# Optimization experiments

Measured on AMD Instinct MI355X. Metric: run time of the kernel, lower is better.

The kernel has to match this reference:

```python
import jax, jax.numpy as jnp
import numpy as np

D_MODEL = 512
N_HEADS = 8
D_FF = 1024
LV = 2048
LT = 512
GAMMA = 0.9
SCALE_BASE = 512  # XPOS default scale_base


def _dup_interleave(m):
    # (L, d/2) -> (L, d) duplicating each column: [a,b] -> [a,a,b,b]
    return jnp.repeat(m, 2, axis=-1)


def _xpos(x, downscale=False):
    # XPOS rotary embedding (RetNet-style), x: (B, L, d)
    B, L, d = x.shape
    half = d // 2
    s = (jnp.arange(0, d, 2, dtype=jnp.float32) + 0.4 * d) / (1.4 * d)  # (d/2,)
    scale = s[None, :] ** (jnp.arange(L, dtype=jnp.float32)[:, None] / SCALE_BASE)  # (L, d/2)
    inv_freq = 1.0 / (10000.0 ** (jnp.arange(half, dtype=jnp.float32) / half))
    ang = jnp.arange(L, dtype=jnp.float32)[:, None] * inv_freq[None, :]  # (L, d/2)
    if downscale:
        scale = 1.0 / scale
    sin = _dup_interleave(jnp.sin(ang) * scale)[None]  # (1, L, d)
    cos = _dup_interleave(jnp.cos(ang) * scale)[None]
    x1, x2 = x[..., 0::2], x[..., 1::2]
    rot = jnp.stack((-x2, x1), axis=-1).reshape(x.shape)  # rotate_every_two
    return x * cos + rot * sin


def _sine_pos(L, d):
    # DETR-style normalized 1D sine position embedding, mask = ones(1, L)
    x_embed = jnp.arange(1, L + 1, dtype=jnp.float32)  # cumsum of ones
    x_embed = x_embed / (x_embed[-1] + 1e-6) * (2.0 * np.pi)
    dim_t = jnp.arange(d, dtype=jnp.float32)
    dim_t = 10000.0 ** (2.0 * jnp.floor(dim_t / 2.0) / d)
    pos = x_embed[:, None] / dim_t[None, :]  # (L, d)
    pos = jnp.stack((jnp.sin(pos[:, 0::2]), jnp.cos(pos[:, 1::2])), axis=2).reshape(L, d)
    return pos[None]  # (1, L, d)


def _ln(x, w, b, eps=1e-5):
    mu = jnp.mean(x, axis=-1, keepdims=True)
    var = jnp.var(x, axis=-1, keepdims=True)
    return (x - mu) / jnp.sqrt(var + eps) * w + b


def _ret_forward(src_vid, src_txt, ln1_w, ln1_b, wq, bq, wk, bk, wv, bv, wo, bo,
                 lin1_w, lin1_b, lin2_w, lin2_b, ln2_w, ln2_b, ln3_w, ln3_b,
                 learn_ret_w):
    B, Lv, D = src_vid.shape
    Lt = src_txt.shape[1]
    h, dk = N_HEADS, D // N_HEADS

    # retention decay matrix D[n,m] = gamma^(n-m) for n>=m else 0
    n = jnp.arange(Lv)
    delta = jnp.maximum(n[:, None] - n[None, :], 0).astype(jnp.float32)
    Dm = jnp.where(n[:, None] >= n[None, :], GAMMA ** delta, 0.0)

    # learned sparse mask
    learn = jax.nn.sigmoid(learn_ret_w.reshape(Lv, Lv))
    diag = jnp.eye(Lv, dtype=jnp.float32)
    video_ret = (1.0 - diag) * learn
    learn_mask = diag + video_ret
    mask = Dm * learn_mask  # mask_choice == 'both'
    loss_sparsity = jnp.mean(jnp.abs(video_ret))

    # position encodings
    pos_vid_q = _xpos(src_vid)
    pos_vid_k = _xpos(src_vid, downscale=True)
    pos_txt = _sine_pos(Lt, D)
    src = jnp.concatenate([src_vid, src_txt], axis=1)       # (B, Lv+Lt, D)
    pos = jnp.concatenate([pos_vid_q, pos_txt], axis=1)
    pos_k = jnp.concatenate([pos_vid_k, pos_txt], axis=1)

    # --- RetLayer (eval mode: dropout = identity) ---
    src2 = _ln(src, ln1_w, ln1_b)
    q = src2[:, :Lv] + pos[:, :Lv]
    k = src2[:, :Lv] + pos_k[:, :Lv]
    v = src2[:, :Lv]

    # multi-head attention with MULTIPLICATIVE mask on logits
    qh = (q @ wq.T + bq).reshape(B, Lv, h, dk) / jnp.sqrt(jnp.float32(dk))
    kh = (k @ wk.T + bk).reshape(B, Lv, h, dk)
    vh = (v @ wv.T + bv).reshape(B, Lv, h, dk)
    attn = jnp.einsum('blhd,bmhd->bhlm', qh, kh) * mask[None, None]
    attn = jax.nn.softmax(attn, axis=-1)
    vid_att = jnp.einsum('bhlm,bmhd->blhd', attn, vh).reshape(B, Lv, D)
    vid_att = vid_att @ wo.T + bo

    src2 = jnp.concatenate([vid_att, src2[:, Lv:]], axis=1) + pos
    src = src + src2
    src2 = _ln(src, ln2_w, ln2_b)
    src2 = jax.nn.gelu(src2 @ lin1_w.T + lin1_b, approximate=False) @ lin2_w.T + lin2_b
    src = src + src2
    src = _ln(src, ln3_w, ln3_b)
    return src[:, :Lv], src[:, Lv:], loss_sparsity


def setup_inputs() -> dict:
    key = jax.random.key(0)
    ks = jax.random.split(key, 12)
    D, F = D_MODEL, D_FF
    w = lambda k, shp: (jax.random.normal(k, shp, dtype=jnp.float32) * 0.02)
    return {
        'src_vid': jax.random.normal(ks[0], (1, LV, D), dtype=jnp.float32),
        'src_txt': jax.random.normal(ks[1], (1, LT, D), dtype=jnp.float32),
        'ln1_w': jnp.ones((D,), jnp.float32), 'ln1_b': jnp.zeros((D,), jnp.float32),
        'wq': w(ks[2], (D, D)), 'bq': jnp.zeros((D,), jnp.float32),
        'wk': w(ks[3], (D, D)), 'bk': jnp.zeros((D,), jnp.float32),
        'wv': w(ks[4], (D, D)), 'bv': jnp.zeros((D,), jnp.float32),
        'wo': w(ks[5], (D, D)), 'bo': jnp.zeros((D,), jnp.float32),
        'lin1_w': w(ks[6], (F, D)), 'lin1_b': jnp.zeros((F,), jnp.float32),
        'lin2_w': w(ks[7], (D, F)), 'lin2_b': jnp.zeros((D,), jnp.float32),
        'ln2_w': jnp.ones((D,), jnp.float32), 'ln2_b': jnp.zeros((D,), jnp.float32),
        'ln3_w': jnp.ones((D,), jnp.float32), 'ln3_b': jnp.zeros((D,), jnp.float32),
        'learn_ret_w': jax.random.normal(ks[8], (LV * LV,), dtype=jnp.float32),
    }


def reference(src_vid, src_txt, ln1_w, ln1_b, wq, bq, wk, bk, wv, bv, wo, bo,
              lin1_w, lin1_b, lin2_w, lin2_b, ln2_w, ln2_b, ln3_w, ln3_b,
              learn_ret_w):
    return _ret_forward(src_vid, src_txt, ln1_w, ln1_b, wq, bq, wk, bk, wv, bv,
                        wo, bo, lin1_w, lin1_b, lin2_w, lin2_b, ln2_w, ln2_b,
                        ln3_w, ln3_b, learn_ret_w)
```

## Files before the change

kernel.cpp:

```cpp
#include <hip/hip_runtime.h>
#include <hip/hip_bf16.h>
#include <math.h>

#define LVID 2048
#define LTXT 512
#define DMOD 512
#define LTOT 2560
#define LOG2_GAMMA (-0.15200309344504995f)
#define LOG2E 1.4426950408889634f

typedef __bf16 bf16x8 __attribute__((ext_vector_type(8)));
typedef float f32x4 __attribute__((ext_vector_type(4)));

__device__ inline f32x4 mfma_bf16(bf16x8 a, bf16x8 b, f32x4 c) {
  return __builtin_amdgcn_mfma_f32_16x16x32_bf16(a, b, c, 0, 0, 0);
}

__device__ inline void gload_lds16(const void* g, void* l) {
  __builtin_amdgcn_global_load_lds(
      (const __attribute__((address_space(1))) void*)g,
      (__attribute__((address_space(3))) void*)l, 16, 0, 0);
}

union U8 { __hip_bfloat16 b[8]; uint4 u; };

__global__ __launch_bounds__(256) void k_prep(
    const float* __restrict__ lw, float* __restrict__ premask2,
    float* __restrict__ loss_out,
    const float* __restrict__ wq, const float* __restrict__ wk,
    const float* __restrict__ wv, const float* __restrict__ wo,
    const float* __restrict__ l1, const float* __restrict__ l2,
    __hip_bfloat16* __restrict__ dst) {
  int tid = threadIdx.x;
  if (blockIdx.x < 2048) {
    __shared__ float red[256];
    int idx0 = (blockIdx.x * 256 + tid) * 8;
    float s = 0.f;
#pragma unroll
    for (int e = 0; e < 8; e++) {
      int idx = idx0 + e;
      int i = idx >> 11, j = idx & 2047;
      float sig = 1.f / (1.f + expf(-lw[idx]));
      if (i != j) s += sig;
      float pm = (j > i) ? 0.f
               : ((j == i) ? 1.f : exp2f((float)(i - j) * LOG2_GAMMA) * sig);
      premask2[idx] = pm * LOG2E;
    }
    red[tid] = s; __syncthreads();
    for (int st = 128; st > 0; st >>= 1) { if (tid < st) red[tid] += red[tid + st]; __syncthreads(); }
    if (tid == 0) atomicAdd(loss_out, red[0] * (1.f / 4194304.f));
  } else {
    int i4 = (blockIdx.x - 2048) * 256 + tid;
    const float* sp; int base;
    if (i4 < 131072)      { if (i4 < 65536)  { sp = wq; base = 0; }      else { sp = wk; base = 65536; } }
    else if (i4 < 262144) { if (i4 < 196608) { sp = wv; base = 131072; } else { sp = wo; base = 196608; } }
    else if (i4 < 393216) { sp = l1; base = 262144; }
    else                  { sp = l2; base = 393216; }
    float4 v = ((const float4*)sp)[i4 - base];
    __hip_bfloat16 o[4] = {__float2bfloat16(v.x), __float2bfloat16(v.y),
                           __float2bfloat16(v.z), __float2bfloat16(v.w)};
    *(uint2*)(dst + (size_t)i4 * 4) = *(uint2*)o;
  }
}

__global__ __launch_bounds__(256) void k_ln1(
    const float* __restrict__ src_vid, const float* __restrict__ src_txt,
    const float* __restrict__ w, const float* __restrict__ b,
    __hip_bfloat16* __restrict__ acat, float* __restrict__ src2f,
    float* __restrict__ posb) {
  int row = blockIdx.x * 4 + (threadIdx.x >> 6);
  int lane = threadIdx.x & 63;
  const float* xs = (row < LVID) ? (src_vid + (size_t)row * DMOD)
                                 : (src_txt + (size_t)(row - LVID) * DMOD);
  float x[8];
  { float4 v0 = *(const float4*)&xs[lane * 8];
    float4 v1 = *(const float4*)&xs[lane * 8 + 4];
    x[0]=v0.x; x[1]=v0.y; x[2]=v0.z; x[3]=v0.w;
    x[4]=v1.x; x[5]=v1.y; x[6]=v1.z; x[7]=v1.w; }
  float s = 0.f;
#pragma unroll
  for (int i = 0; i < 8; i++) s += x[i];
#pragma unroll
  for (int st = 1; st < 64; st <<= 1) s += __shfl_xor(s, st, 64);
  float mu = s * (1.f / DMOD);
  float vs = 0.f;
#pragma unroll
  for (int i = 0; i < 8; i++) { float d = x[i] - mu; vs += d * d; }
#pragma unroll
  for (int st = 1; st < 64; st <<= 1) vs += __shfl_xor(vs, st, 64);
  float inv = rsqrtf(vs * (1.f / DMOD) + 1e-5f);
  float y[8];
  { float4 w0 = *(const float4*)&w[lane * 8];
    float4 w1 = *(const float4*)&w[lane * 8 + 4];
    float4 b0 = *(const float4*)&b[lane * 8];
    float4 b1 = *(const float4*)&b[lane * 8 + 4];
    float wv_[8] = {w0.x,w0.y,w0.z,w0.w,w1.x,w1.y,w1.z,w1.w};
    float bv_[8] = {b0.x,b0.y,b0.z,b0.w,b1.x,b1.y,b1.z,b1.w};
#pragma unroll
    for (int i = 0; i < 8; i++) y[i] = (x[i] - mu) * inv * wv_[i] + bv_[i]; }
  size_t base = (size_t)row * DMOD + lane * 8;
  if (row < LVID) {
    U8 pv;
#pragma unroll
    for (int i = 0; i < 8; i++) pv.b[i] = __float2bfloat16(y[i]);
    *(uint4*)&acat[(size_t)(4096 + row) * DMOD + lane * 8] = pv.u;
    float pq[8], pk[8];
    float l = (float)row;
#pragma unroll
    for (int p = 0; p < 4; p++) {
      int j = lane * 4 + p;
      float sj = (2.f * j + 204.8f) * (1.f / 716.8f);
      float scale = powf(sj, l * (1.f / 512.f));
      float invfreq = powf(10000.f, -(float)j * (1.f / 256.f));
      float sn, cs; sincosf(l * invfreq, &sn, &cs);
      float cq = cs * scale, sq = sn * scale;
      pq[2*p]   = x[2*p] * cq - x[2*p+1] * sq;
      pq[2*p+1] = x[2*p+1] * cq + x[2*p] * sq;
      float isc = 1.f / scale;
      float ck = cs * isc, sk = sn * isc;
      pk[2*p]   = x[2*p] * ck - x[2*p+1] * sk;
      pk[2*p+1] = x[2*p+1] * ck + x[2*p] * sk;
    }
    *(float4*)&posb[base]     = *(float4*)&pq[0];
    *(float4*)&posb[base + 4] = *(float4*)&pq[4];
    U8 pqv, pkv;
#pragma unroll
    for (int i = 0; i < 8; i++) {
      pqv.b[i] = __float2bfloat16(y[i] + pq[i]);
      pkv.b[i] = __float2bfloat16(y[i] + pk[i]);
    }
    *(uint4*)&acat[(size_t)row * DMOD + lane * 8] = pqv.u;
    *(uint4*)&acat[(size_t)(2048 + row) * DMOD + lane * 8] = pkv.u;
  } else {
    *(float4*)&src2f[base]     = *(float4*)&y[0];
    *(float4*)&src2f[base + 4] = *(float4*)&y[4];
    int l = row - LVID;
    float xe = (float)(l + 1) * (6.28318530717958647692f / 512.000001f);
    float ps[8];
#pragma unroll
    for (int p = 0; p < 4; p++) {
      int j = lane * 4 + p;
      float dimt = powf(10000.f, (float)j * (1.f / 256.f));
      float a = xe / dimt;
      ps[2*p] = sinf(a); ps[2*p+1] = cosf(a);
    }
    *(float4*)&posb[base]     = *(float4*)&ps[0];
    *(float4*)&posb[base + 4] = *(float4*)&ps[4];
  }
}

__global__ __launch_bounds__(256) void k_ln2(
    const float* __restrict__ src_txt, const float* __restrict__ src2f,
    const float* __restrict__ posb, float* __restrict__ srcA,
    const float* __restrict__ w, const float* __restrict__ b,
    __hip_bfloat16* __restrict__ obf) {
  int row = blockIdx.x * 4 + (threadIdx.x >> 6);
  int lane = threadIdx.x & 63;
  size_t base = (size_t)row * DMOD + lane * 8;
  float x[8];
  if (row < LVID) {
    float4 v0 = *(const float4*)&srcA[base];
    float4 v1 = *(const float4*)&srcA[base + 4];
    x[0]=v0.x; x[1]=v0.y; x[2]=v0.z; x[3]=v0.w;
    x[4]=v1.x; x[5]=v1.y; x[6]=v1.z; x[7]=v1.w;
  } else {
    size_t tb = (size_t)(row - LVID) * DMOD + lane * 8;
#pragma unroll
    for (int i = 0; i < 8; i++) x[i] = src_txt[tb + i] + src2f[base + i] + posb[base + i];
    *(float4*)&srcA[base]     = *(float4*)&x[0];
    *(float4*)&srcA[base + 4] = *(float4*)&x[4];
  }
  float s = 0.f;
#pragma unroll
  for (int i = 0; i < 8; i++) s += x[i];
#pragma unroll
  for (int st = 1; st < 64; st <<= 1) s += __shfl_xor(s, st, 64);
  float mu = s * (1.f / DMOD);
  float vs = 0.f;
#pragma unroll
  for (int i = 0; i < 8; i++) { float d = x[i] - mu; vs += d * d; }
#pragma unroll
  for (int st = 1; st < 64; st <<= 1) vs += __shfl_xor(vs, st, 64);
  float inv = rsqrtf(vs * (1.f / DMOD) + 1e-5f);
  float4 w0 = *(const float4*)&w[lane * 8];
  float4 w1 = *(const float4*)&w[lane * 8 + 4];
  float4 b0 = *(const float4*)&b[lane * 8];
  float4 b1 = *(const float4*)&b[lane * 8 + 4];
  float wv_[8] = {w0.x,w0.y,w0.z,w0.w,w1.x,w1.y,w1.z,w1.w};
  float bv_[8] = {b0.x,b0.y,b0.z,b0.w,b1.x,b1.y,b1.z,b1.w};
  U8 o;
#pragma unroll
  for (int i = 0; i < 8; i++)
    o.b[i] = __float2bfloat16((x[i] - mu) * inv * wv_[i] + bv_[i]);
  *(uint4*)&obf[base] = o.u;
}

__global__ __launch_bounds__(256) void k_ln3(
    const float* __restrict__ srcA, const float* __restrict__ ffo,
    const float* __restrict__ w, const float* __restrict__ b,
    float* __restrict__ o) {
  int row = blockIdx.x * 4 + (threadIdx.x >> 6);
  int lane = threadIdx.x & 63;
  size_t base = (size_t)row * DMOD + lane * 8;
  float x[8];
  { float4 a0 = *(const float4*)&srcA[base];
    float4 a1 = *(const float4*)&srcA[base + 4];
    float4 f0 = *(const float4*)&ffo[base];
    float4 f1 = *(const float4*)&ffo[base + 4];
    x[0]=a0.x+f0.x; x[1]=a0.y+f0.y; x[2]=a0.z+f0.z; x[3]=a0.w+f0.w;
    x[4]=a1.x+f1.x; x[5]=a1.y+f1.y; x[6]=a1.z+f1.z; x[7]=a1.w+f1.w; }
  float s = 0.f;
#pragma unroll
  for (int i = 0; i < 8; i++) s += x[i];
#pragma unroll
  for (int st = 1; st < 64; st <<= 1) s += __shfl_xor(s, st, 64);
  float mu = s * (1.f / DMOD);
  float vs = 0.f;
#pragma unroll
  for (int i = 0; i < 8; i++) { float d = x[i] - mu; vs += d * d; }
#pragma unroll
  for (int st = 1; st < 64; st <<= 1) vs += __shfl_xor(vs, st, 64);
  float inv = rsqrtf(vs * (1.f / DMOD) + 1e-5f);
  float4 w0 = *(const float4*)&w[lane * 8];
  float4 w1 = *(const float4*)&w[lane * 8 + 4];
  float4 b0 = *(const float4*)&b[lane * 8];
  float4 b1 = *(const float4*)&b[lane * 8 + 4];
  float wv_[8] = {w0.x,w0.y,w0.z,w0.w,w1.x,w1.y,w1.z,w1.w};
  float bv_[8] = {b0.x,b0.y,b0.z,b0.w,b1.x,b1.y,b1.z,b1.w};
  float y[8];
#pragma unroll
  for (int i = 0; i < 8; i++) y[i] = (x[i] - mu) * inv * wv_[i] + bv_[i];
  *(float4*)&o[base]     = *(float4*)&y[0];
  *(float4*)&o[base + 4] = *(float4*)&y[4];
}

template <int EPI>
__global__ __launch_bounds__(256) void k_gemm2(
    const __hip_bfloat16* __restrict__ A, const __hip_bfloat16* __restrict__ W0,
    const float* __restrict__ b0, const float* __restrict__ b1,
    const float* __restrict__ b2, void* __restrict__ Cv,
    const float* __restrict__ res1, const float* __restrict__ res2,
    float* __restrict__ vtot, int M, int N, int K) {
  __shared__ __hip_bfloat16 sA[2][4096];
  __shared__ __hip_bfloat16 sB[2][4096];
  int tid = threadIdx.x, lane = tid & 63, w = tid >> 6;
  int c16 = lane & 15, q4 = lane >> 4;
  int bm = blockIdx.y * 64, bn = blockIdx.x * 64;
  int seg = (EPI == 3) ? (bm >> 11) : 0;
  const __hip_bfloat16* Wp = (EPI == 3) ? (W0 + (size_t)seg * N * K) : W0;
  int srow = tid >> 2, scol = (tid & 3) * 8;
  const __hip_bfloat16* gA = A + (size_t)(bm + srow) * K + scol;
  const __hip_bfloat16* gB = Wp + (size_t)(bn + srow) * K + scol;
  auto stage = [&](int buf, int k0) {
    gload_lds16(gA + k0,      &sA[buf][0]    + (size_t)tid * 8);
    gload_lds16(gA + k0 + 32, &sA[buf][2048] + (size_t)tid * 8);
    gload_lds16(gB + k0,      &sB[buf][0]    + (size_t)tid * 8);
    gload_lds16(gB + k0 + 32, &sB[buf][2048] + (size_t)tid * 8);
  };
  f32x4 acc[2][2];
  { f32x4 z = {0.f,0.f,0.f,0.f}; acc[0][0]=z; acc[0][1]=z; acc[1][0]=z; acc[1][1]=z; }
  int wm = w & 1, wn = w >> 1;
  const int S = K >> 6;
  stage(0, 0);
  for (int s = 0; s < S; s++) {
    __syncthreads();
    if (s + 1 < S) stage((s + 1) & 1, (s + 1) * 64);
    int bf = s & 1;
#pragma unroll
    for (int kc = 0; kc < 2; kc++) {
      bf16x8 a0  = *(const bf16x8*)&sA[bf][kc*2048 + (wm*32 + c16)*32 + q4*8];
      bf16x8 a1  = *(const bf16x8*)&sA[bf][kc*2048 + (wm*32 + 16 + c16)*32 + q4*8];
      bf16x8 bv0 = *(const bf16x8*)&sB[bf][kc*2048 + (wn*32 + c16)*32 + q4*8];
      bf16x8 bv1 = *(const bf16x8*)&sB[bf][kc*2048 + (wn*32 + 16 + c16)*32 + q4*8];
      acc[0][0] = mfma_bf16(a0, bv0, acc[0][0]);
      acc[0][1] = mfma_bf16(a0, bv1, acc[0][1]);
      acc[1][0] = mfma_bf16(a1, bv0, acc[1][0]);
      acc[1][1] = mfma_bf16(a1, bv1, acc[1][1]);
    }
  }
  float alpha = (EPI == 3 && seg == 0) ? 0.125f : 1.f;
  const float* bp = (EPI == 3) ? (seg == 0 ? b0 : (seg == 1 ? b1 : b2)) : b0;
  float vsum[2] = {0.f, 0.f};
#pragma unroll
  for (int t = 0; t < 2; t++) {
#pragma unroll
    for (int u = 0; u < 2; u++) {
      int n = bn + wn*32 + u*16 + c16;
      float bs = bp[n];
#pragma unroll
      for (int r = 0; r < 4; r++) {
        int m = bm + wm*32 + t*16 + q4*4 + r;
        float v = (acc[t][u][r] + bs) * alpha;
        if (EPI == 4) v = 0.5f * v * (1.f + erff(v * 0.70710678118654752f));
        if (EPI == 0) {
          ((float*)Cv)[(size_t)m * N + n] = v;
        } else if (EPI == 1 || EPI == 4) {
          ((__hip_bfloat16*)Cv)[(size_t)m * N + n] = __float2bfloat16(v);
        } else if (EPI == 2) {
          size_t off = (size_t)m * N + n;
          ((float*)Cv)[off] = v + res1[off] + res2[off];
        } else {
          __hip_bfloat16 vb = __float2bfloat16(v);
          ((__hip_bfloat16*)Cv)[(size_t)(m & 2047) * 1536 + seg * 512 + n] = vb;
          if (seg == 2) vsum[u] += __bfloat162float(vb);
        }
      }
    }
  }
  if (EPI == 3 && seg == 2) {
#pragma unroll
    for (int u = 0; u < 2; u++) {
      float s2 = vsum[u];
      s2 += __shfl_xor(s2, 16, 64);
      s2 += __shfl_xor(s2, 32, 64);
      if (q4 == 0) atomicAdd(&vtot[bn + wn*32 + u*16 + c16], s2);
    }
  }
}

__global__ __launch_bounds__(256) void k_attn(
    const __hip_bfloat16* __restrict__ qkv,
    const float* __restrict__ premask2,
    const float* __restrict__ Vtot,
    __hip_bfloat16* __restrict__ outp) {
  __shared__ __hip_bfloat16 sQ[64][72];
  __shared__ __hip_bfloat16 sK[2][64][72];
  __shared__ __hip_bfloat16 sVt[2][64][72];
  __shared__ __hip_bfloat16 sP[64][72];
  __shared__ float sVa[4][64];
  int i0 = blockIdx.x * 64, h = blockIdx.y;
  int tid = threadIdx.x, lane = tid & 63, w = tid >> 6;
  int c16 = lane & 15, q4 = lane >> 4;
  {
    int r = tid >> 2, c0 = (tid & 3) * 16;
    const __hip_bfloat16* g = qkv + (size_t)(i0 + r) * 1536 + h * 64 + c0;
    *(uint4*)&sQ[r][c0]     = *(const uint4*)g;
    *(uint4*)&sQ[r][c0 + 8] = *(const uint4*)(g + 8);
  }
  int thi = i0 >> 6;
  int tlo = (i0 > 900) ? ((i0 - 900) >> 6) : 0;
  float rm = 0.f, rz = 0.f;
  f32x4 O[4];
  { f32x4 z = {0.f,0.f,0.f,0.f}; O[0]=z; O[1]=z; O[2]=z; O[3]=z; }
  float vacc = 0.f;
  int kr = tid >> 2, kc = (tid & 3) * 16;
  uint4 pk0, pk1;
  U8 pv0, pv1;
  {
    const __hip_bfloat16* gk = qkv + (size_t)(tlo*64 + kr) * 1536 + 512 + h*64 + kc;
    pk0 = *(const uint4*)gk; pk1 = *(const uint4*)(gk + 8);
    const __hip_bfloat16* gv = qkv + (size_t)(tlo*64 + w*16) * 1536 + 1024 + h*64 + lane;
#pragma unroll
    for (int j = 0; j < 8; j++) pv0.b[j] = gv[(size_t)j * 1536];
#pragma unroll
    for (int j = 0; j < 8; j++) pv1.b[j] = gv[(size_t)(j + 8) * 1536];
  }
  for (int t = tlo; t <= thi; t++) {
    int buf = (t - tlo) & 1;
    *(uint4*)&sK[buf][kr][kc]       = pk0;
    *(uint4*)&sK[buf][kr][kc + 8]   = pk1;
    *(uint4*)&sVt[buf][lane][w*16]     = pv0.u;
    *(uint4*)&sVt[buf][lane][w*16 + 8] = pv1.u;
#pragma unroll
    for (int j = 0; j < 8; j++) vacc += __bfloat162float(pv0.b[j]);
#pragma unroll
    for (int j = 0; j < 8; j++) vacc += __bfloat162float(pv1.b[j]);
    __syncthreads();
    if (t < thi) {
      const __hip_bfloat16* gk = qkv + (size_t)((t+1)*64 + kr) * 1536 + 512 + h*64 + kc;
      pk0 = *(const uint4*)gk; pk1 = *(const uint4*)(gk + 8);
      const __hip_bfloat16* gv = qkv + (size_t)((t+1)*64 + w*16) * 1536 + 1024 + h*64 + lane;
#pragma unroll
      for (int j = 0; j < 8; j++) pv0.b[j] = gv[(size_t)j * 1536];
#pragma unroll
      for (int j = 0; j < 8; j++) pv1.b[j] = gv[(size_t)(j + 8) * 1536];
    }
    bf16x8 bq0 = *(const bf16x8*)&sQ[w*16 + c16][q4*8];
    bf16x8 bq1 = *(const bf16x8*)&sQ[w*16 + c16][32 + q4*8];
    f32x4 St[4];
#pragma unroll
    for (int jt = 0; jt < 4; jt++) {
      f32x4 z = {0.f,0.f,0.f,0.f};
      bf16x8 a0 = *(const bf16x8*)&sK[buf][jt*16 + c16][q4*8];
      bf16x8 a1 = *(const bf16x8*)&sK[buf][jt*16 + c16][32 + q4*8];
      z = mfma_bf16(a0, bq0, z);
      z = mfma_bf16(a1, bq1, z);
      St[jt] = z;
    }
    int qg = i0 + w*16 + c16;
    float lg[4][4];
    float tmax = -3.0e38f;
#pragma unroll
    for (int jt = 0; jt < 4; jt++) {
      float4 pm = *(const float4*)&premask2[(size_t)qg * 2048 + t*64 + jt*16 + q4*4];
      lg[jt][0] = St[jt][0] * pm.x; lg[jt][1] = St[jt][1] * pm.y;
      lg[jt][2] = St[jt][2] * pm.z; lg[jt][3] = St[jt][3] * pm.w;
#pragma unroll
      for (int r = 0; r < 4; r++) tmax = fmaxf(tmax, lg[jt][r]);
    }
    tmax = fmaxf(tmax, __shfl_xor(tmax, 16, 64));
    tmax = fmaxf(tmax, __shfl_xor(tmax, 32, 64));
    float mn = fmaxf(rm, tmax);
    float al = exp2f(rm - mn);
    rm = mn;
    float zp = 0.f;
#pragma unroll
    for (int jt = 0; jt < 4; jt++) {
      U8 e4;
      float e0 = exp2f(lg[jt][0] - rm), e1 = exp2f(lg[jt][1] - rm);
      float e2 = exp2f(lg[jt][2] - rm), e3 = exp2f(lg[jt][3] - rm);
      zp += e0 + e1 + e2 + e3;
      e4.b[0] = __float2bfloat16(e0); e4.b[1] = __float2bfloat16(e1);
      e4.b[2] = __float2bfloat16(e2); e4.b[3] = __float2bfloat16(e3);
      *(uint2*)&sP[w*16 + c16][jt*16 + q4*4] = *(uint2*)&e4.b[0];
    }
    zp += __shfl_xor(zp, 16, 64);
    zp += __shfl_xor(zp, 32, 64);
    rz = rz * al + zp;
    float alr[4];
#pragma unroll
    for (int r = 0; r < 4; r++) alr[r] = __shfl(al, q4*4 + r, 64);
#pragma unroll
    for (int dt = 0; dt < 4; dt++)
#pragma unroll
      for (int r = 0; r < 4; r++) O[dt][r] *= alr[r];
    bf16x8 ap0 = *(const bf16x8*)&sP[w*16 + c16][q4*8];
    bf16x8 ap1 = *(const bf16x8*)&sP[w*16 + c16][32 + q4*8];
#pragma unroll
    for (int dt = 0; dt < 4; dt++) {
      bf16x8 bv0 = *(const bf16x8*)&sVt[buf][dt*16 + c16][q4*8];
      bf16x8 bv1 = *(const bf16x8*)&sVt[buf][dt*16 + c16][32 + q4*8];
      O[dt] = mfma_bf16(ap0, bv0, O[dt]);
      O[dt] = mfma_bf16(ap1, bv1, O[dt]);
    }
  }
  sVa[w][lane] = vacc;
  __syncthreads();
  float rmr[4], rzr[4];
#pragma unroll
  for (int r = 0; r < 4; r++) {
    rmr[r] = __shfl(rm, q4*4 + r, 64);
    rzr[r] = __shfl(rz, q4*4 + r, 64);
  }
  float nu = (float)(2048 - 64 * (thi - tlo + 1));
#pragma unroll
  for (int dt = 0; dt < 4; dt++) {
    int d = dt*16 + c16;
    float va = sVa[0][d] + sVa[1][d] + sVa[2][d] + sVa[3][d];
    float vu = Vtot[h*64 + d] - va;
#pragma unroll
    for (int r = 0; r < 4; r++) {
      float eu = exp2f(-rmr[r]);
      float o = (O[dt][r] + eu * vu) / (rzr[r] + nu * eu);
      outp[(size_t)(i0 + w*16 + q4*4 + r) * DMOD + h*64 + d] = __float2bfloat16(o);
    }
  }
}

extern "C" void kernel_launch(void* const* d_in, const int* in_sizes, int n_in,
                              void* d_out, int out_size, void* d_ws, size_t ws_size,
                              hipStream_t stream) {
  const float* src_vid = (const float*)d_in[0];
  const float* src_txt = (const float*)d_in[1];
  const float* ln1_w = (const float*)d_in[2];
  const float* ln1_b = (const float*)d_in[3];
  const float* wq = (const float*)d_in[4];
  const float* bq = (const float*)d_in[5];
  const float* wk = (const float*)d_in[6];
  const float* bk = (const float*)d_in[7];
  const float* wv = (const float*)d_in[8];
  const float* bv = (const float*)d_in[9];
  const float* wo = (const float*)d_in[10];
  const float* bo = (const float*)d_in[11];
  const float* lin1_w = (const float*)d_in[12];
  const float* lin1_b = (const float*)d_in[13];
  const float* lin2_w = (const float*)d_in[14];
  const float* lin2_b = (const float*)d_in[15];
  const float* ln2_w = (const float*)d_in[16];
  const float* ln2_b = (const float*)d_in[17];
  const float* ln3_w = (const float*)d_in[18];
  const float* ln3_b = (const float*)d_in[19];
  const float* lw = (const float*)d_in[20];
  float* out = (float*)d_out;

  char* wsb = (char*)d_ws;
  float* premask2       = (float*)(wsb + 0);
  __hip_bfloat16* wqb   = (__hip_bfloat16*)(wsb + 16777216);
  __hip_bfloat16* wob   = wqb + 786432;
  __hip_bfloat16* l1b   = wqb + 1048576;
  __hip_bfloat16* l2b   = wqb + 1572864;
  __hip_bfloat16* acat  = (__hip_bfloat16*)(wsb + 20971520);
  __hip_bfloat16* qkvb  = (__hip_bfloat16*)(wsb + 27262976);
  __hip_bfloat16* vattb = (__hip_bfloat16*)(wsb + 33554432);
  float* srcA           = (float*)(wsb + 35651584);
  float* src2f          = (float*)(wsb + 40894464);
  float* posb           = (float*)(wsb + 46137344);
  __hip_bfloat16* s2b   = (__hip_bfloat16*)(wsb + 51380224);
  __hip_bfloat16* hidb  = (__hip_bfloat16*)(wsb + 54525952);
  float* ffo            = (float*)(wsb + 59768832);
  float* Vtot           = (float*)(wsb + 65011712);

  hipMemsetAsync(out + 1310720, 0, sizeof(float), stream);
  hipMemsetAsync(Vtot, 0, 512 * sizeof(float), stream);

  k_prep<<<4096, 256, 0, stream>>>(lw, premask2, out + 1310720,
                                   wq, wk, wv, wo, lin1_w, lin2_w, wqb);
  k_ln1<<<640, 256, 0, stream>>>(src_vid, src_txt, ln1_w, ln1_b,
                                 acat, src2f, posb);
  k_gemm2<3><<<dim3(8, 96), 256, 0, stream>>>(acat, wqb, bq, bk, bv,
      qkvb, nullptr, nullptr, Vtot, 6144, 512, 512);
  k_attn<<<dim3(32, 8), 256, 0, stream>>>(qkvb, premask2, Vtot, vattb);
  k_gemm2<2><<<dim3(8, 32), 256, 0, stream>>>(vattb, wob, bo, nullptr, nullptr,
      srcA, src_vid, posb, nullptr, 2048, 512, 512);
  k_ln2<<<640, 256, 0, stream>>>(src_txt, src2f, posb, srcA, ln2_w, ln2_b, s2b);
  k_gemm2<4><<<dim3(16, 40), 256, 0, stream>>>(s2b, l1b, lin1_b, nullptr, nullptr,
      hidb, nullptr, nullptr, nullptr, 2560, 1024, 512);
  k_gemm2<0><<<dim3(8, 40), 256, 0, stream>>>(hidb, l2b, lin2_b, nullptr, nullptr,
      ffo, nullptr, nullptr, nullptr, 2560, 512, 1024);
  k_ln3<<<640, 256, 0, stream>>>(srcA, ffo, ln3_w, ln3_b, out);
}
```

Baseline: 238.3 us.

## Enlarge GEMM tiles to 128x128, fuse prep with LN1, use fast math

The GEMM block tile grows from 64x64 to 128x128 with a 4x4 MFMA accumulator per wave and a k-step of 32, so each staged fragment is reused more and fewer blocks are launched. The prep and LN1 kernels are merged into one launch, and the loss is accumulated in workspace and copied to the output in LN3, which removes one memset. Transcendentals switch to fast intrinsics (__expf, __powf, __sincosf). The risks are low occupancy from grids of only 64-192 blocks on a large GPU, more register pressure, and lower accuracy in the positional terms.

```diff
diff --git a/kernel.cpp b/kernel.cpp
--- a/kernel.cpp
+++ b/kernel.cpp
@@ -24,23 +24,28 @@
 
 union U8 { __hip_bfloat16 b[8]; uint4 u; };
 
-__global__ __launch_bounds__(256) void k_prep(
+__global__ __launch_bounds__(256) void k_prep_ln1(
     const float* __restrict__ lw, float* __restrict__ premask2,
-    float* __restrict__ loss_out,
+    float* __restrict__ lossws,
     const float* __restrict__ wq, const float* __restrict__ wk,
     const float* __restrict__ wv, const float* __restrict__ wo,
     const float* __restrict__ l1, const float* __restrict__ l2,
-    __hip_bfloat16* __restrict__ dst) {
+    __hip_bfloat16* __restrict__ dst,
+    const float* __restrict__ src_vid, const float* __restrict__ src_txt,
+    const float* __restrict__ w, const float* __restrict__ b,
+    __hip_bfloat16* __restrict__ acat, float* __restrict__ src2f,
+    float* __restrict__ posb) {
   int tid = threadIdx.x;
-  if (blockIdx.x < 2048) {
+  int blk = blockIdx.x;
+  if (blk < 2048) {
     __shared__ float red[256];
-    int idx0 = (blockIdx.x * 256 + tid) * 8;
+    int idx0 = (blk * 256 + tid) * 8;
     float s = 0.f;
 #pragma unroll
     for (int e = 0; e < 8; e++) {
       int idx = idx0 + e;
       int i = idx >> 11, j = idx & 2047;
-      float sig = 1.f / (1.f + expf(-lw[idx]));
+      float sig = 1.f / (1.f + __expf(-lw[idx]));
       if (i != j) s += sig;
       float pm = (j > i) ? 0.f
                : ((j == i) ? 1.f : exp2f((float)(i - j) * LOG2_GAMMA) * sig);
@@ -48,9 +53,9 @@
     }
     red[tid] = s; __syncthreads();
     for (int st = 128; st > 0; st >>= 1) { if (tid < st) red[tid] += red[tid + st]; __syncthreads(); }
-    if (tid == 0) atomicAdd(loss_out, red[0] * (1.f / 4194304.f));
-  } else {
-    int i4 = (blockIdx.x - 2048) * 256 + tid;
+    if (tid == 0) atomicAdd(lossws, red[0] * (1.f / 4194304.f));
+  } else if (blk < 4096) {
+    int i4 = (blk - 2048) * 256 + tid;
     const float* sp; int base;
     if (i4 < 131072)      { if (i4 < 65536)  { sp = wq; base = 0; }      else { sp = wk; base = 65536; } }
     else if (i4 < 262144) { if (i4 < 196608) { sp = wv; base = 131072; } else { sp = wo; base = 196608; } }
@@ -60,92 +65,86 @@
     __hip_bfloat16 o[4] = {__float2bfloat16(v.x), __float2bfloat16(v.y),
                            __float2bfloat16(v.z), __float2bfloat16(v.w)};
     *(uint2*)(dst + (size_t)i4 * 4) = *(uint2*)o;
-  }
-}
-
-__global__ __launch_bounds__(256) void k_ln1(
-    const float* __restrict__ src_vid, const float* __restrict__ src_txt,
-    const float* __restrict__ w, const float* __restrict__ b,
-    __hip_bfloat16* __restrict__ acat, float* __restrict__ src2f,
-    float* __restrict__ posb) {
-  int row = blockIdx.x * 4 + (threadIdx.x >> 6);
-  int lane = threadIdx.x & 63;
-  const float* xs = (row < LVID) ? (src_vid + (size_t)row * DMOD)
-                                 : (src_txt + (size_t)(row - LVID) * DMOD);
-  float x[8];
-  { float4 v0 = *(const float4*)&xs[lane * 8];
-    float4 v1 = *(const float4*)&xs[lane * 8 + 4];
-    x[0]=v0.x; x[1]=v0.y; x[2]=v0.z; x[3]=v0.w;
-    x[4]=v1.x; x[5]=v1.y; x[6]=v1.z; x[7]=v1.w; }
-  float s = 0.f;
-#pragma unroll
-  for (int i = 0; i < 8; i++) s += x[i];
-#pragma unroll
-  for (int st = 1; st < 64; st <<= 1) s += __shfl_xor(s, st, 64);
-  float mu = s * (1.f / DMOD);
-  float vs = 0.f;
-#pragma unroll
-  for (int i = 0; i < 8; i++) { float d = x[i] - mu; vs += d * d; }
-#pragma unroll
-  for (int st = 1; st < 64; st <<= 1) vs += __shfl_xor(vs, st, 64);
-  float inv = rsqrtf(vs * (1.f / DMOD) + 1e-5f);
-  float y[8];
-  { float4 w0 = *(const float4*)&w[lane * 8];
-    float4 w1 = *(const float4*)&w[lane * 8 + 4];
-    float4 b0 = *(const float4*)&b[lane * 8];
-    float4 b1 = *(const float4*)&b[lane * 8 + 4];
-    float wv_[8] = {w0.x,w0.y,w0.z,w0.w,w1.x,w1.y,w1.z,w1.w};
-    float bv_[8] = {b0.x,b0.y,b0.z,b0.w,b1.x,b1.y,b1.z,b1.w};
-#pragma unroll
-    for (int i = 0; i < 8; i++) y[i] = (x[i] - mu) * inv * wv_[i] + bv_[i]; }
-  size_t base = (size_t)row * DMOD + lane * 8;
-  if (row < LVID) {
-    U8 pv;
-#pragma unroll
-    for (int i = 0; i < 8; i++) pv.b[i] = __float2bfloat16(y[i]);
-    *(uint4*)&acat[(size_t)(4096 + row) * DMOD + lane * 8] = pv.u;
-    float pq[8], pk[8];
-    float l = (float)row;
-#pragma unroll
-    for (int p = 0; p < 4; p++) {
-      int j = lane * 4 + p;
-      float sj = (2.f * j + 204.8f) * (1.f / 716.8f);
-      float scale = powf(sj, l * (1.f / 512.f));
-      float invfreq = powf(10000.f, -(float)j * (1.f / 256.f));
-      float sn, cs; sincosf(l * invfreq, &sn, &cs);
-      float cq = cs * scale, sq = sn * scale;
-      pq[2*p]   = x[2*p] * cq - x[2*p+1] * sq;
-      pq[2*p+1] = x[2*p+1] * cq + x[2*p] * sq;
-      float isc = 1.f / scale;
-      float ck = cs * isc, sk = sn * isc;
-      pk[2*p]   = x[2*p] * ck - x[2*p+1] * sk;
-      pk[2*p+1] = x[2*p+1] * ck + x[2*p] * sk;
-    }
-    *(float4*)&posb[base]     = *(float4*)&pq[0];
-    *(float4*)&posb[base + 4] = *(float4*)&pq[4];
-    U8 pqv, pkv;
-#pragma unroll
-    for (int i = 0; i < 8; i++) {
-      pqv.b[i] = __float2bfloat16(y[i] + pq[i]);
-      pkv.b[i] = __float2bfloat16(y[i] + pk[i]);
-    }
-    *(uint4*)&acat[(size_t)row * DMOD + lane * 8] = pqv.u;
-    *(uint4*)&acat[(size_t)(2048 + row) * DMOD + lane * 8] = pkv.u;
   } else {
-    *(float4*)&src2f[base]     = *(float4*)&y[0];
-    *(float4*)&src2f[base + 4] = *(float4*)&y[4];
-    int l = row - LVID;
-    float xe = (float)(l + 1) * (6.28318530717958647692f / 512.000001f);
-    float ps[8];
-#pragma unroll
-    for (int p = 0; p < 4; p++) {
-      int j = lane * 4 + p;
-      float dimt = powf(10000.f, (float)j * (1.f / 256.f));
-      float a = xe / dimt;
-      ps[2*p] = sinf(a); ps[2*p+1] = cosf(a);
-    }
-    *(float4*)&posb[base]     = *(float4*)&ps[0];
-    *(float4*)&posb[base + 4] = *(float4*)&ps[4];
+    int row = (blk - 4096) * 4 + (tid >> 6);
+    int lane = tid & 63;
+    const float* xs = (row < LVID) ? (src_vid + (size_t)row * DMOD)
+                                   : (src_txt + (size_t)(row - LVID) * DMOD);
+    float x[8];
+    { float4 v0 = *(const float4*)&xs[lane * 8];
+      float4 v1 = *(const float4*)&xs[lane * 8 + 4];
+      x[0]=v0.x; x[1]=v0.y; x[2]=v0.z; x[3]=v0.w;
+      x[4]=v1.x; x[5]=v1.y; x[6]=v1.z; x[7]=v1.w; }
+    float s = 0.f;
+#pragma unroll
+    for (int i = 0; i < 8; i++) s += x[i];
+#pragma unroll
+    for (int st = 1; st < 64; st <<= 1) s += __shfl_xor(s, st, 64);
+    float mu = s * (1.f / DMOD);
+    float vs = 0.f;
+#pragma unroll
+    for (int i = 0; i < 8; i++) { float d = x[i] - mu; vs += d * d; }
+#pragma unroll
+    for (int st = 1; st < 64; st <<= 1) vs += __shfl_xor(vs, st, 64);
+    float inv = rsqrtf(vs * (1.f / DMOD) + 1e-5f);
+    float y[8];
+    { float4 w0 = *(const float4*)&w[lane * 8];
+      float4 w1 = *(const float4*)&w[lane * 8 + 4];
+      float4 b0 = *(const float4*)&b[lane * 8];
+      float4 b1 = *(const float4*)&b[lane * 8 + 4];
+      float wv_[8] = {w0.x,w0.y,w0.z,w0.w,w1.x,w1.y,w1.z,w1.w};
+      float bv_[8] = {b0.x,b0.y,b0.z,b0.w,b1.x,b1.y,b1.z,b1.w};
+#pragma unroll
+      for (int i = 0; i < 8; i++) y[i] = (x[i] - mu) * inv * wv_[i] + bv_[i]; }
+    size_t base = (size_t)row * DMOD + lane * 8;
+    if (row < LVID) {
+      U8 pv;
+#pragma unroll
+      for (int i = 0; i < 8; i++) pv.b[i] = __float2bfloat16(y[i]);
+      *(uint4*)&acat[(size_t)(4096 + row) * DMOD + lane * 8] = pv.u;
+      float pq[8], pk[8];
+      float l = (float)row;
+#pragma unroll
+      for (int p = 0; p < 4; p++) {
+        int j = lane * 4 + p;
+        float sj = (2.f * j + 204.8f) * (1.f / 716.8f);
+        float scale = __powf(sj, l * (1.f / 512.f));
+        float invfreq = __powf(10000.f, -(float)j * (1.f / 256.f));
+        float sn, cs; __sincosf(l * invfreq, &sn, &cs);
+        float cq = cs * scale, sq = sn * scale;
+        pq[2*p]   = x[2*p] * cq - x[2*p+1] * sq;
+        pq[2*p+1] = x[2*p+1] * cq + x[2*p] * sq;
+        float isc = 1.f / scale;
+        float ck = cs * isc, sk = sn * isc;
+        pk[2*p]   = x[2*p] * ck - x[2*p+1] * sk;
+        pk[2*p+1] = x[2*p+1] * ck + x[2*p] * sk;
+      }
+      *(float4*)&posb[base]     = *(float4*)&pq[0];
+      *(float4*)&posb[base + 4] = *(float4*)&pq[4];
+      U8 pqv, pkv;
+#pragma unroll
+      for (int i = 0; i < 8; i++) {
+        pqv.b[i] = __float2bfloat16(y[i] + pq[i]);
+        pkv.b[i] = __float2bfloat16(y[i] + pk[i]);
+      }
+      *(uint4*)&acat[(size_t)row * DMOD + lane * 8] = pqv.u;
+      *(uint4*)&acat[(size_t)(2048 + row) * DMOD + lane * 8] = pkv.u;
+    } else {
+      *(float4*)&src2f[base]     = *(float4*)&y[0];
+      *(float4*)&src2f[base + 4] = *(float4*)&y[4];
+      int l = row - LVID;
+      float xe = (float)(l + 1) * (6.28318530717958647692f / 512.000001f);
+      float ps[8];
+#pragma unroll
+      for (int p = 0; p < 4; p++) {
+        int j = lane * 4 + p;
+        float dimt = __powf(10000.f, (float)j * (1.f / 256.f));
+        float a = xe / dimt;
+        ps[2*p] = __sinf(a); ps[2*p+1] = __cosf(a);
+      }
+      *(float4*)&posb[base]     = *(float4*)&ps[0];
+      *(float4*)&posb[base + 4] = *(float4*)&ps[4];
+    }
   }
 }
 
@@ -198,7 +197,8 @@
 __global__ __launch_bounds__(256) void k_ln3(
     const float* __restrict__ srcA, const float* __restrict__ ffo,
     const float* __restrict__ w, const float* __restrict__ b,
-    float* __restrict__ o) {
+    float* __restrict__ o, const float* __restrict__ lossws) {
+  if (blockIdx.x == 0 && threadIdx.x == 0) o[1310720] = lossws[0];
   int row = blockIdx.x * 4 + (threadIdx.x >> 6);
   int lane = threadIdx.x & 63;
   size_t base = (size_t)row * DMOD + lane * 8;
@@ -235,7 +235,7 @@
 }
 
 template <int EPI>
-__global__ __launch_bounds__(256) void k_gemm2(
+__global__ __launch_bounds__(256) void k_gemm3(
     const __hip_bfloat16* __restrict__ A, const __hip_bfloat16* __restrict__ W0,
     const float* __restrict__ b0, const float* __restrict__ b1,
     const float* __restrict__ b2, void* __restrict__ Cv,
@@ -245,75 +245,82 @@
   __shared__ __hip_bfloat16 sB[2][4096];
   int tid = threadIdx.x, lane = tid & 63, w = tid >> 6;
   int c16 = lane & 15, q4 = lane >> 4;
-  int bm = blockIdx.y * 64, bn = blockIdx.x * 64;
+  int bm = blockIdx.y * 128, bn = blockIdx.x * 128;
   int seg = (EPI == 3) ? (bm >> 11) : 0;
-  const __hip_bfloat16* Wp = (EPI == 3) ? (W0 + (size_t)seg * N * K) : W0;
-  int srow = tid >> 2, scol = (tid & 3) * 8;
-  const __hip_bfloat16* gA = A + (size_t)(bm + srow) * K + scol;
-  const __hip_bfloat16* gB = Wp + (size_t)(bn + srow) * K + scol;
+  const __hip_bfloat16* Wp = (EPI == 3) ? (W0 + (size_t)seg * ((size_t)N * K)) : W0;
+  int r0 = tid >> 2, cc0 = (tid & 3) * 8;
+  const __hip_bfloat16* gA0 = A  + (size_t)(bm + r0) * K + cc0;
+  const __hip_bfloat16* gA1 = A  + (size_t)(bm + 64 + r0) * K + cc0;
+  const __hip_bfloat16* gB0 = Wp + (size_t)(bn + r0) * K + cc0;
+  const __hip_bfloat16* gB1 = Wp + (size_t)(bn + 64 + r0) * K + cc0;
   auto stage = [&](int buf, int k0) {
-    gload_lds16(gA + k0,      &sA[buf][0]    + (size_t)tid * 8);
-    gload_lds16(gA + k0 + 32, &sA[buf][2048] + (size_t)tid * 8);
-    gload_lds16(gB + k0,      &sB[buf][0]    + (size_t)tid * 8);
-    gload_lds16(gB + k0 + 32, &sB[buf][2048] + (size_t)tid * 8);
+    gload_lds16(gA0 + k0, &sA[buf][(size_t)tid * 8]);
+    gload_lds16(gA1 + k0, &sA[buf][2048 + (size_t)tid * 8]);
+    gload_lds16(gB0 + k0, &sB[buf][(size_t)tid * 8]);
+    gload_lds16(gB1 + k0, &sB[buf][2048 + (size_t)tid * 8]);
   };
-  f32x4 acc[2][2];
-  { f32x4 z = {0.f,0.f,0.f,0.f}; acc[0][0]=z; acc[0][1]=z; acc[1][0]=z; acc[1][1]=z; }
+  f32x4 acc[4][4];
+  { f32x4 z = {0.f,0.f,0.f,0.f};
+#pragma unroll
+    for (int i = 0; i < 4; i++)
+#pragma unroll
+      for (int j = 0; j < 4; j++) acc[i][j] = z; }
   int wm = w & 1, wn = w >> 1;
-  const int S = K >> 6;
+  const int S = K >> 5;
   stage(0, 0);
   for (int s = 0; s < S; s++) {
     __syncthreads();
-    if (s + 1 < S) stage((s + 1) & 1, (s + 1) * 64);
+    if (s + 1 < S) stage((s + 1) & 1, (s + 1) * 32);
     int bf = s & 1;
-#pragma unroll
-    for (int kc = 0; kc < 2; kc++) {
-      bf16x8 a0  = *(const bf16x8*)&sA[bf][kc*2048 + (wm*32 + c16)*32 + q4*8];
-      bf16x8 a1  = *(const bf16x8*)&sA[bf][kc*2048 + (wm*32 + 16 + c16)*32 + q4*8];
-      bf16x8 bv0 = *(const bf16x8*)&sB[bf][kc*2048 + (wn*32 + c16)*32 + q4*8];
-      bf16x8 bv1 = *(const bf16x8*)&sB[bf][kc*2048 + (wn*32 + 16 + c16)*32 + q4*8];
-      acc[0][0] = mfma_bf16(a0, bv0, acc[0][0]);
-      acc[0][1] = mfma_bf16(a0, bv1, acc[0][1]);
-      acc[1][0] = mfma_bf16(a1, bv0, acc[1][0]);
-      acc[1][1] = mfma_bf16(a1, bv1, acc[1][1]);
-    }
+    bf16x8 af[4], bfr[4];
+#pragma unroll
+    for (int i = 0; i < 4; i++)
+      af[i] = *(const bf16x8*)&sA[bf][(wm*64 + i*16 + c16) * 32 + q4*8];
+#pragma unroll
+    for (int j = 0; j < 4; j++)
+      bfr[j] = *(const bf16x8*)&sB[bf][(wn*64 + j*16 + c16) * 32 + q4*8];
+#pragma unroll
+    for (int i = 0; i < 4; i++)
+#pragma unroll
+      for (int j = 0; j < 4; j++)
+        acc[i][j] = mfma_bf16(af[i], bfr[j], acc[i][j]);
   }
   float alpha = (EPI == 3 && seg == 0) ? 0.125f : 1.f;
   const float* bp = (EPI == 3) ? (seg == 0 ? b0 : (seg == 1 ? b1 : b2)) : b0;
-  float vsum[2] = {0.f, 0.f};
-#pragma unroll
-  for (int t = 0; t < 2; t++) {
-#pragma unroll
-    for (int u = 0; u < 2; u++) {
-      int n = bn + wn*32 + u*16 + c16;
-      float bs = bp[n];
+  float vsum[4] = {0.f, 0.f, 0.f, 0.f};
+#pragma unroll
+  for (int j = 0; j < 4; j++) {
+    int n = bn + wn*64 + j*16 + c16;
+    float bs = bp[n];
+#pragma unroll
+    for (int i = 0; i < 4; i++) {
 #pragma unroll
       for (int r = 0; r < 4; r++) {
-        int m = bm + wm*32 + t*16 + q4*4 + r;
-        float v = (acc[t][u][r] + bs) * alpha;
+        int m = bm + wm*64 + i*16 + q4*4 + r;
+        float v = (acc[i][j][r] + bs) * alpha;
         if (EPI == 4) v = 0.5f * v * (1.f + erff(v * 0.70710678118654752f));
         if (EPI == 0) {
           ((float*)Cv)[(size_t)m * N + n] = v;
-        } else if (EPI == 1 || EPI == 4) {
-          ((__hip_bfloat16*)Cv)[(size_t)m * N + n] = __float2bfloat16(v);
         } else if (EPI == 2) {
           size_t off = (size_t)m * N + n;
           ((float*)Cv)[off] = v + res1[off] + res2[off];
+        } else if (EPI == 4) {
+          ((__hip_bfloat16*)Cv)[(size_t)m * N + n] = __float2bfloat16(v);
         } else {
           __hip_bfloat16 vb = __float2bfloat16(v);
           ((__hip_bfloat16*)Cv)[(size_t)(m & 2047) * 1536 + seg * 512 + n] = vb;
-          if (seg == 2) vsum[u] += __bfloat162float(vb);
+          if (seg == 2) vsum[j] += __bfloat162float(vb);
         }
       }
     }
   }
   if (EPI == 3 && seg == 2) {
 #pragma unroll
-    for (int u = 0; u < 2; u++) {
-      float s2 = vsum[u];
+    for (int j = 0; j < 4; j++) {
+      float s2 = vsum[j];
       s2 += __shfl_xor(s2, 16, 64);
       s2 += __shfl_xor(s2, 32, 64);
-      if (q4 == 0) atomicAdd(&vtot[bn + wn*32 + u*16 + c16], s2);
+      if (q4 == 0) atomicAdd(&vtot[bn + wn*64 + j*16 + c16], s2);
     }
   }
 }
@@ -499,23 +506,23 @@
   __hip_bfloat16* hidb  = (__hip_bfloat16*)(wsb + 54525952);
   float* ffo            = (float*)(wsb + 59768832);
   float* Vtot           = (float*)(wsb + 65011712);
-
-  hipMemsetAsync(out + 1310720, 0, sizeof(float), stream);
-  hipMemsetAsync(Vtot, 0, 512 * sizeof(float), stream);
-
-  k_prep<<<4096, 256, 0, stream>>>(lw, premask2, out + 1310720,
-                                   wq, wk, wv, wo, lin1_w, lin2_w, wqb);
-  k_ln1<<<640, 256, 0, stream>>>(src_vid, src_txt, ln1_w, ln1_b,
-                                 acat, src2f, posb);
-  k_gemm2<3><<<dim3(8, 96), 256, 0, stream>>>(acat, wqb, bq, bk, bv,
+  float* lossws         = Vtot + 512;
+
+  hipMemsetAsync(Vtot, 0, 513 * sizeof(float), stream);
+
+  k_prep_ln1<<<4736, 256, 0, stream>>>(lw, premask2, lossws,
+      wq, wk, wv, wo, lin1_w, lin2_w, wqb,
+      src_vid, src_txt, ln1_w, ln1_b, acat, src2f, posb);
+
+  k_gemm3<3><<<dim3(4, 48), 256, 0, stream>>>(acat, wqb, bq, bk, bv,
       qkvb, nullptr, nullptr, Vtot, 6144, 512, 512);
   k_attn<<<dim3(32, 8), 256, 0, stream>>>(qkvb, premask2, Vtot, vattb);
-  k_gemm2<2><<<dim3(8, 32), 256, 0, stream>>>(vattb, wob, bo, nullptr, nullptr,
+  k_gemm3<2><<<dim3(4, 16), 256, 0, stream>>>(vattb, wob, bo, nullptr, nullptr,
       srcA, src_vid, posb, nullptr, 2048, 512, 512);
   k_ln2<<<640, 256, 0, stream>>>(src_txt, src2f, posb, srcA, ln2_w, ln2_b, s2b);
-  k_gemm2<4><<<dim3(16, 40), 256, 0, stream>>>(s2b, l1b, lin1_b, nullptr, nullptr,
+  k_gemm3<4><<<dim3(8, 20), 256, 0, stream>>>(s2b, l1b, lin1_b, nullptr, nullptr,
       hidb, nullptr, nullptr, nullptr, 2560, 1024, 512);
-  k_gemm2<0><<<dim3(8, 40), 256, 0, stream>>>(hidb, l2b, lin2_b, nullptr, nullptr,
+  k_gemm3<0><<<dim3(4, 20), 256, 0, stream>>>(hidb, l2b, lin2_b, nullptr, nullptr,
       ffo, nullptr, nullptr, nullptr, 2560, 512, 1024);
-  k_ln3<<<640, 256, 0, stream>>>(srcA, ffo, ln3_w, ln3_b, out);
-}
+  k_ln3<<<640, 256, 0, stream>>>(srcA, ffo, ln3_w, ln3_b, out, lossws);
+}
```

Result: slower. 262.4 us (+10.1%).
